# Kernel tuning notes

Hardware: AMD Instinct MI355X
Metric: run time of the kernel (lower is better)

The kernel has to match this reference:

```python
import jax, jax.numpy as jnp
import numpy as np

D_MODEL, N_HEADS, D_K, D_V, D_FF, SEQ = 2048, 16, 128, 128, 8192, 2048
EPS = 1e-5


def _layernorm(x, g, b):
    mu = jnp.mean(x, axis=-1, keepdims=True)
    var = jnp.var(x, axis=-1, keepdims=True)
    return (x - mu) * jax.lax.rsqrt(var + EPS) * g + b


def setup_inputs() -> dict:
    key = jax.random.key(0)
    ks = jax.random.split(key, 10)
    return {
        "x": jax.random.normal(ks[0], (SEQ, D_MODEL), jnp.float32),
        # per-head projections stacked over heads (matches num_heads separate DotProductAttention params)
        "wq": jax.random.normal(ks[1], (N_HEADS, D_MODEL, D_K), jnp.float32),
        "wk": jax.random.normal(ks[2], (N_HEADS, D_MODEL, D_K), jnp.float32),
        "wv": jax.random.normal(ks[3], (N_HEADS, D_MODEL, D_V), jnp.float32),
        "w_proj": jax.random.normal(ks[4], (N_HEADS * D_V, D_MODEL), jnp.float32),
        "g1": jnp.ones((D_MODEL,), jnp.float32),
        "b1": jnp.zeros((D_MODEL,), jnp.float32),
        "fc1_w": jax.random.normal(ks[5], (D_MODEL, D_FF), jnp.float32) * 0.02,
        "fc1_b": jnp.zeros((D_FF,), jnp.float32),
        "fc2_w": jax.random.normal(ks[6], (D_FF, D_MODEL), jnp.float32) * 0.02,
        "fc2_b": jnp.zeros((D_MODEL,), jnp.float32),
        "g2": jnp.ones((D_MODEL,), jnp.float32),
        "b2": jnp.zeros((D_MODEL,), jnp.float32),
    }


def reference(x, wq, wk, wv, w_proj, g1, b1, fc1_w, fc1_b, fc2_w, fc2_b, g2, b2):
    # multi-head attention (heads batched via einsum; same math as the per-head loop)
    q = jnp.einsum("sd,hdk->hsk", x, wq)
    k = jnp.einsum("sd,hdk->hsk", x, wk)
    v = jnp.einsum("sd,hdv->hsv", x, wv)
    scores = jnp.einsum("hsk,htk->hst", q, k) * (1.0 / np.sqrt(D_K))
    attn = jax.nn.softmax(scores, axis=-1)
    heads = jnp.einsum("hst,htv->hsv", attn, v)  # [H,S,Dv]
    concat = jnp.transpose(heads, (1, 0, 2)).reshape(SEQ, N_HEADS * D_V)
    attn_out = concat @ w_proj
    # residual + LayerNorm (dropout=0 -> identity)
    h = _layernorm(x + attn_out, g1, b1)
    # FFN with ReLU
    ff = jax.nn.relu(h @ fc1_w + fc1_b) @ fc2_w + fc2_b
    return _layernorm(h + ff, g2, b2)
```

## Files before the change

### kernel.cpp

```cpp
#include <hip/hip_runtime.h>


typedef __bf16 bf16;
typedef __attribute__((ext_vector_type(8))) __bf16 bf16x8;
typedef __attribute__((ext_vector_type(4))) __bf16 bf16x4;
typedef __attribute__((ext_vector_type(4))) float f32x4;

#define MFMA(a, b, c) __builtin_amdgcn_mfma_f32_16x16x32_bf16((a), (b), (c), 0, 0, 0)
#define NEG_INF (-3.402823466e38f)

__device__ __forceinline__ void cp16(void* lds, const void* g) {
  __builtin_amdgcn_global_load_lds(
      (const __attribute__((address_space(1))) unsigned int*)g,
      (__attribute__((address_space(3))) unsigned int*)lds, 16, 0, 0);
}

#define SBAR() __builtin_amdgcn_sched_barrier(0)
#define GBAR()                              \
  do {                                      \
    asm volatile("" ::: "memory");          \
    __builtin_amdgcn_s_barrier();           \
    asm volatile("" ::: "memory");          \
  } while (0)
#define LGKM0()                                         \
  do {                                                  \
    asm volatile("s_waitcnt lgkmcnt(0)" ::: "memory");  \
    __builtin_amdgcn_sched_barrier(0);                  \
  } while (0)
#define VMC6()                                          \
  do {                                                  \
    asm volatile("s_waitcnt vmcnt(6)" ::: "memory");    \
    __builtin_amdgcn_sched_barrier(0);                  \
  } while (0)


__global__ void k_split_x(const float* __restrict__ x, bf16* __restrict__ xh,
                          bf16* __restrict__ xl) {
  int i = blockIdx.x * 256 + threadIdx.x;
  f32x4 v = ((const f32x4*)x)[i];
  bf16x4 h, l;
#pragma unroll
  for (int j = 0; j < 4; ++j) {
    bf16 hi = (bf16)v[j];
    h[j] = hi;
    l[j] = (bf16)(v[j] - (float)hi);
  }
  ((bf16x4*)xh)[i] = h;
  ((bf16x4*)xl)[i] = l;
}

template <bool SPLIT>
__global__ void k_tcvt(const float* __restrict__ in, bf16* __restrict__ oh,
                       bf16* __restrict__ ol, int R, int C) {
  __shared__ float t[64][65];
  long zoff = (long)blockIdx.z * R * C;
  int c0 = blockIdx.x * 64, r0 = blockIdx.y * 64;
  int cc = threadIdx.x & 63, rr = threadIdx.x >> 6;
#pragma unroll
  for (int i = 0; i < 16; ++i) {
    int r = i * 4 + rr;
    t[r][cc] = in[zoff + (long)(r0 + r) * C + c0 + cc];
  }
  __syncthreads();
#pragma unroll
  for (int i = 0; i < 16; ++i) {
    int orow = i * 4 + rr;
    float v = t[cc][orow];
    long oidx = zoff + (long)(c0 + orow) * R + r0 + cc;
    bf16 hi = (bf16)v;
    oh[oidx] = hi;
    if (SPLIT) ol[oidx] = (bf16)(v - (float)hi);
  }
}

__global__ void k_combine4(const float* __restrict__ p, long pstr,
                           bf16* __restrict__ o) {
  int i = blockIdx.x * 256 + threadIdx.x;
  f32x4 v = ((const f32x4*)p)[i];
#pragma unroll
  for (int zz = 1; zz < 4; ++zz) v += ((const f32x4*)(p + zz * pstr))[i];
  bf16x4 ob;
#pragma unroll
  for (int j = 0; j < 4; ++j) ob[j] = (bf16)v[j];
  ((bf16x4*)o)[i] = ob;
}

template <int EPI>
__global__ __launch_bounds__(512, 1) void k_gemm8(
    const bf16* __restrict__ A, const bf16* __restrict__ B,
    float* __restrict__ Cf, bf16* __restrict__ Cb,
    const float* __restrict__ bias, int M, int N, int K, int nsplit) {
  __shared__ char lds[131072];
  const int tid = threadIdx.x, w = tid >> 6, l = tid & 63;
  const int l16 = l & 15, lg = l >> 4;
  const int wr = w >> 2, wc = w & 3;
  const long bm0 = (long)blockIdx.y * 256, bn0 = (long)blockIdx.x * 256;
  const int z = blockIdx.z;
  const int ksz = K / nsplit, kbeg = z * ksz;
  const int nt = ksz >> 6;
  const long lK = K;

  const int srow = w * 8 + (l >> 3);
  const int sslot = (l & 7) ^ (l >> 3);

  auto STAGE = [&](int bufp, int isB, int h, int tt) {
    int tc = tt < nt ? tt : nt - 1;
    char* dst = lds + bufp * 65536 + isB * 32768 + h * 16384 + w * 1024;
    const bf16* G = isB ? B : A;
    long r0 = (isB ? bn0 : bm0) + h * 128 + srow;
    const bf16* src = G + r0 * lK + kbeg + tc * 64 + sslot * 8;
    cp16(dst, src);
    cp16(dst + 8192, src + 64 * lK);
  };
  auto LDA = [&](int bufp, int mf, int ks) -> bf16x8 {
    int inrow = (mf & 3) * 32 + wr * 16 + l16;
    int byo = bufp * 65536 + (mf >> 2) * 16384 + inrow * 128 +
              ((((ks << 2) + lg) ^ (inrow & 7)) << 4);
    return *(const bf16x8*)(lds + byo);
  };
  auto LDB = [&](int bufp, int nf, int ks) -> bf16x8 {
    int inrow = (nf & 1) * 64 + wc * 16 + l16;
    int byo = bufp * 65536 + 32768 + (nf >> 1) * 16384 + inrow * 128 +
              ((((ks << 2) + lg) ^ (inrow & 7)) << 4);
    return *(const bf16x8*)(lds + byo);
  };

  f32x4 acc[8][4];
#pragma unroll
  for (int mf = 0; mf < 8; ++mf)
#pragma unroll
    for (int nf = 0; nf < 4; ++nf)
#pragma unroll
      for (int j = 0; j < 4; ++j) acc[mf][nf][j] = 0.f;

  STAGE(0, 0, 0, 0);
  STAGE(0, 1, 0, 0);
  STAGE(0, 0, 1, 0);
  STAGE(0, 1, 1, 0);
  STAGE(1, 1, 0, 1);
  STAGE(1, 0, 1, 1);
  STAGE(1, 1, 1, 1);
  SBAR();
  VMC6();
  GBAR();

  bf16x8 a[4][2], b[2][2];
  for (int t = 0; t < nt; ++t) {
    const int cb = t & 1, nb = cb ^ 1;
#pragma unroll
    for (int mf = 0; mf < 4; ++mf)
#pragma unroll
      for (int ks = 0; ks < 2; ++ks) a[mf][ks] = LDA(cb, mf, ks);
#pragma unroll
    for (int nf = 0; nf < 2; ++nf)
#pragma unroll
      for (int ks = 0; ks < 2; ++ks) b[nf][ks] = LDB(cb, nf, ks);
    STAGE(nb, 0, 0, t + 1);
    SBAR();
    GBAR();
    LGKM0();
    __builtin_amdgcn_s_setprio(1);
#pragma unroll
    for (int mf = 0; mf < 4; ++mf)
#pragma unroll
      for (int nf = 0; nf < 2; ++nf)
#pragma unroll
        for (int ks = 0; ks < 2; ++ks)
          acc[mf][nf] = MFMA(a[mf][ks], b[nf][ks], acc[mf][nf]);
    __builtin_amdgcn_s_setprio(0);
    GBAR();
#pragma unroll
    for (int mf = 0; mf < 4; ++mf)
#pragma unroll
      for (int ks = 0; ks < 2; ++ks) a[mf][ks] = LDA(cb, mf + 4, ks);
    STAGE(cb, 1, 0, t + 2);
    SBAR();
    GBAR();
    LGKM0();
    __builtin_amdgcn_s_setprio(1);
#pragma unroll
    for (int mf = 0; mf < 4; ++mf)
#pragma unroll
      for (int nf = 0; nf < 2; ++nf)
#pragma unroll
        for (int ks = 0; ks < 2; ++ks)
          acc[mf + 4][nf] = MFMA(a[mf][ks], b[nf][ks], acc[mf + 4][nf]);
    __builtin_amdgcn_s_setprio(0);
    GBAR();
#pragma unroll
    for (int nf = 0; nf < 2; ++nf)
#pragma unroll
      for (int ks = 0; ks < 2; ++ks) b[nf][ks] = LDB(cb, nf + 2, ks);
    GBAR();
    LGKM0();
    __builtin_amdgcn_s_setprio(1);
#pragma unroll
    for (int mf = 0; mf < 4; ++mf)
#pragma unroll
      for (int nf = 0; nf < 2; ++nf)
#pragma unroll
        for (int ks = 0; ks < 2; ++ks)
          acc[mf + 4][nf + 2] = MFMA(a[mf][ks], b[nf][ks], acc[mf + 4][nf + 2]);
    __builtin_amdgcn_s_setprio(0);
    GBAR();
#pragma unroll
    for (int mf = 0; mf < 4; ++mf)
#pragma unroll
      for (int ks = 0; ks < 2; ++ks) a[mf][ks] = LDA(cb, mf, ks);
    STAGE(cb, 0, 1, t + 2);
    STAGE(cb, 1, 1, t + 2);
    SBAR();
    VMC6();
    GBAR();
    LGKM0();
    __builtin_amdgcn_s_setprio(1);
#pragma unroll
    for (int mf = 0; mf < 4; ++mf)
#pragma unroll
      for (int nf = 0; nf < 2; ++nf)
#pragma unroll
        for (int ks = 0; ks < 2; ++ks)
          acc[mf][nf + 2] = MFMA(a[mf][ks], b[nf][ks], acc[mf][nf + 2]);
    __builtin_amdgcn_s_setprio(0);
    GBAR();
  }
  asm volatile("s_waitcnt vmcnt(0) lgkmcnt(0)" ::: "memory");

#pragma unroll
  for (int mf = 0; mf < 8; ++mf)
#pragma unroll
    for (int nf = 0; nf < 4; ++nf) {
      long col = bn0 + nf * 64 + wc * 16 + l16;
      float bv = (EPI == 2) ? bias[col] : 0.f;
#pragma unroll
      for (int jj = 0; jj < 4; ++jj) {
        long row = bm0 + mf * 32 + wr * 16 + lg * 4 + jj;
        float v = acc[mf][nf][jj];
        if (EPI == 0) {
          Cf[(long)z * M * N + row * N + col] = v;
        } else {
          v = fmaxf(v + bv, 0.f);
          Cb[row * N + col] = (bf16)v;
        }
      }
    }
}

__global__ __launch_bounds__(512, 1) void k_split8(
    const bf16* __restrict__ Ah_g, const bf16* __restrict__ Al_g,
    const bf16* __restrict__ Bh_g, const bf16* __restrict__ Bl_g,
    bf16* __restrict__ Ch, bf16* __restrict__ Cl,
    int M, int N, int K, float scale, int scale_ncols) {
  __shared__ char lds[98304];
  const int tid = threadIdx.x, w = tid >> 6, l = tid & 63;
  const int l16 = l & 15, lg = l >> 4;
  const int wr = w >> 2, wc = w & 3;
  const long bm0 = (long)blockIdx.y * 128, bn0 = (long)blockIdx.x * 256;
  const int nt = K >> 5;
  const long lK = K;

  const int srcrow = tid >> 2;
  const int ss = (tid & 3) ^ ((tid >> 3) & 3);

  auto STG_A = [&](int bufp, int isLo, int tt) {
    int tc = tt < nt ? tt : nt - 1;
    char* dst = lds + bufp * 49152 + isLo * 8192 + tid * 16;
    const bf16* G = isLo ? Al_g : Ah_g;
    cp16(dst, &G[(bm0 + srcrow) * lK + tc * 32 + ss * 8]);
  };
  auto STG_B = [&](int bufp, int isLo, int half, int tt) {
    int tc = tt < nt ? tt : nt - 1;
    char* dst = lds + bufp * 49152 + 16384 + isLo * 16384 + half * 8192 + tid * 16;
    const bf16* G = isLo ? Bl_g : Bh_g;
    cp16(dst, &G[(bn0 + half * 128 + srcrow) * lK + tc * 32 + ss * 8]);
  };
  auto LDA8 = [&](int bufp, int mf, int isLo) -> bf16x8 {
    int row = mf * 32 + wr * 16 + l16;
    int byo = bufp * 49152 + isLo * 8192 + row * 64 +
              ((lg ^ ((row >> 1) & 3)) << 4);
    return *(const bf16x8*)(lds + byo);
  };
  auto LDB8 = [&](int bufp, int nf, int isLo) -> bf16x8 {
    int row = nf * 64 + wc * 16 + l16;
    int byo = bufp * 49152 + 16384 + isLo * 16384 + row * 64 +
              ((lg ^ ((row >> 1) & 3)) << 4);
    return *(const bf16x8*)(lds + byo);
  };

  f32x4 acc[4][4];
#pragma unroll
  for (int mf = 0; mf < 4; ++mf)
#pragma unroll
    for (int nf = 0; nf < 4; ++nf)
#pragma unroll
      for (int j = 0; j < 4; ++j) acc[mf][nf][j] = 0.f;

  STG_B(0, 0, 0, 0); STG_B(0, 1, 0, 0);
  STG_A(0, 0, 0);    STG_A(0, 1, 0);
  STG_B(0, 0, 1, 0); STG_B(0, 1, 1, 0);
  STG_B(1, 0, 0, 1); STG_B(1, 1, 0, 1);
  STG_A(1, 0, 1);    STG_A(1, 1, 1);
  STG_B(1, 0, 1, 1); STG_B(1, 1, 1, 1);
  SBAR();
  VMC6();
  GBAR();

  bf16x8 ah[4], al[4], bh[2], bl[2];
  for (int t = 0; t < nt; ++t) {
    const int cb = t & 1;
#pragma unroll
    for (int mf = 0; mf < 2; ++mf) {
      ah[mf] = LDA8(cb, mf, 0);
      al[mf] = LDA8(cb, mf, 1);
    }
#pragma unroll
    for (int nf = 0; nf < 2; ++nf) {
      bh[nf] = LDB8(cb, nf, 0);
      bl[nf] = LDB8(cb, nf, 1);
    }
    SBAR();
    GBAR();
    LGKM0();
    __builtin_amdgcn_s_setprio(1);
#pragma unroll
    for (int mf = 0; mf < 2; ++mf)
#pragma unroll
      for (int nf = 0; nf < 2; ++nf) {
        acc[mf][nf] = MFMA(ah[mf], bh[nf], acc[mf][nf]);
        acc[mf][nf] = MFMA(ah[mf], bl[nf], acc[mf][nf]);
        acc[mf][nf] = MFMA(al[mf], bh[nf], acc[mf][nf]);
      }
    __builtin_amdgcn_s_setprio(0);
    GBAR();
#pragma unroll
    for (int mf = 2; mf < 4; ++mf) {
      ah[mf] = LDA8(cb, mf, 0);
      al[mf] = LDA8(cb, mf, 1);
    }
    STG_B(cb, 0, 0, t + 2);
    STG_B(cb, 1, 0, t + 2);
    SBAR();
    GBAR();
    LGKM0();
    __builtin_amdgcn_s_setprio(1);
#pragma unroll
    for (int mf = 2; mf < 4; ++mf)
#pragma unroll
      for (int nf = 0; nf < 2; ++nf) {
        acc[mf][nf] = MFMA(ah[mf], bh[nf], acc[mf][nf]);
        acc[mf][nf] = MFMA(ah[mf], bl[nf], acc[mf][nf]);
        acc[mf][nf] = MFMA(al[mf], bh[nf], acc[mf][nf]);
      }
    __builtin_amdgcn_s_setprio(0);
    GBAR();
#pragma unroll
    for (int nf = 0; nf < 2; ++nf) {
      bh[nf] = LDB8(cb, nf + 2, 0);
      bl[nf] = LDB8(cb, nf + 2, 1);
    }
    STG_A(cb, 0, t + 2);
    STG_A(cb, 1, t + 2);
    SBAR();
    GBAR();
    LGKM0();
    __builtin_amdgcn_s_setprio(1);
#pragma unroll
    for (int mf = 2; mf < 4; ++mf)
#pragma unroll
      for (int nf = 0; nf < 2; ++nf) {
        acc[mf][nf + 2] = MFMA(ah[mf], bh[nf], acc[mf][nf + 2]);
        acc[mf][nf + 2] = MFMA(ah[mf], bl[nf], acc[mf][nf + 2]);
        acc[mf][nf + 2] = MFMA(al[mf], bh[nf], acc[mf][nf + 2]);
      }
    __builtin_amdgcn_s_setprio(0);
    GBAR();
    STG_B(cb, 0, 1, t + 2);
    STG_B(cb, 1, 1, t + 2);
    SBAR();
    VMC6();
    GBAR();
    __builtin_amdgcn_s_setprio(1);
#pragma unroll
    for (int mf = 0; mf < 2; ++mf)
#pragma unroll
      for (int nf = 0; nf < 2; ++nf) {
        acc[mf][nf + 2] = MFMA(ah[mf], bh[nf], acc[mf][nf + 2]);
        acc[mf][nf + 2] = MFMA(ah[mf], bl[nf], acc[mf][nf + 2]);
        acc[mf][nf + 2] = MFMA(al[mf], bh[nf], acc[mf][nf + 2]);
      }
    __builtin_amdgcn_s_setprio(0);
    GBAR();
  }
  asm volatile("s_waitcnt vmcnt(0) lgkmcnt(0)" ::: "memory");

#pragma unroll
  for (int mf = 0; mf < 4; ++mf)
#pragma unroll
    for (int nf = 0; nf < 4; ++nf) {
      long col = bn0 + nf * 64 + wc * 16 + l16;
      float sc = (col < scale_ncols) ? scale : 1.0f;
#pragma unroll
      for (int j = 0; j < 4; ++j) {
        long row = bm0 + mf * 32 + wr * 16 + lg * 4 + j;
        float v = acc[mf][nf][j] * sc;
        bf16 hi = (bf16)v;
        Ch[row * N + col] = hi;
        Cl[row * N + col] = (bf16)(v - (float)hi);
      }
    }
}

__global__ __launch_bounds__(256, 3) void k_flash(
    const bf16* __restrict__ Qh, const bf16* __restrict__ Ql,
    const bf16* __restrict__ Kh, const bf16* __restrict__ Kl,
    const bf16* __restrict__ Vt, bf16* __restrict__ Oc) {
  __shared__ bf16 sm[24576];
  bf16* sKh = sm;
  bf16* sKl = sm + 8192;
  bf16* sVt = sm + 16384;
  bf16* sP = sKl;
  const int tid = threadIdx.x, w = tid >> 6, l = tid & 63;
  const int l16 = l & 15, lg = l >> 4;
  const int head = blockIdx.y;
  const long q0 = (long)blockIdx.x * 64;

  bf16x8 qh_r[4], ql_r[4];
#pragma unroll
  for (int kk = 0; kk < 4; ++kk) {
    long off = (q0 + w * 16 + l16) * 4096 + head * 128 + kk * 32 + lg * 8;
    qh_r[kk] = *(const bf16x8*)&Qh[off];
    ql_r[kk] = *(const bf16x8*)&Ql[off];
  }

  f32x4 acc_o[8];
#pragma unroll
  for (int n = 0; n < 8; ++n)
#pragma unroll
    for (int j = 0; j < 4; ++j) acc_o[n][j] = 0.f;
  float mrow[4], lrow[4];
#pragma unroll
  for (int j = 0; j < 4; ++j) {
    mrow[j] = NEG_INF;
    lrow[j] = 0.f;
  }

  for (int t0 = 0; t0 < 2048; t0 += 64) {
    __syncthreads();
#pragma unroll
    for (int i = 0; i < 4; ++i) {
      int c = (w * 4 + i) * 64 + l;
      int rk = c >> 4, sk = (c & 15) ^ (rk & 7);
      long ko = (long)(t0 + rk) * 4096 + head * 128 + sk * 8;
      int db = (w * 4 + i) * 512;
      cp16(&sKh[db], &Kh[ko]);
      cp16(&sKl[db], &Kl[ko]);
      int rv = c >> 3, sv = (c & 7) ^ (rv & 7);
      long vo = (long)(head * 128 + rv) * 2048 + t0 + sv * 8;
      cp16(&sVt[db], &Vt[vo]);
    }
    __syncthreads();

    f32x4 s[4];
#pragma unroll
    for (int n = 0; n < 4; ++n)
#pragma unroll
      for (int j = 0; j < 4; ++j) s[n][j] = 0.f;
    __builtin_amdgcn_s_setprio(1);
#pragma unroll
    for (int kk = 0; kk < 4; ++kk) {
      bf16x8 bh[4], bl[4];
#pragma unroll
      for (int n = 0; n < 4; ++n) {
        int r = n * 16 + l16;
        int byo = r * 256 + (((kk * 4 + lg) ^ (r & 7)) << 4);
        bh[n] = *(const bf16x8*)((const char*)sKh + byo);
        bl[n] = *(const bf16x8*)((const char*)sKl + byo);
      }
#pragma unroll
      for (int n = 0; n < 4; ++n) {
        s[n] = MFMA(qh_r[kk], bh[n], s[n]);
        s[n] = MFMA(qh_r[kk], bl[n], s[n]);
        s[n] = MFMA(ql_r[kk], bh[n], s[n]);
      }
    }
    __builtin_amdgcn_s_setprio(0);
    __syncthreads();

#pragma unroll
    for (int j = 0; j < 4; ++j) {
      float mx = fmaxf(fmaxf(s[0][j], s[1][j]), fmaxf(s[2][j], s[3][j]));
      mx = fmaxf(mx, __shfl_xor(mx, 1));
      mx = fmaxf(mx, __shfl_xor(mx, 2));
      mx = fmaxf(mx, __shfl_xor(mx, 4));
      mx = fmaxf(mx, __shfl_xor(mx, 8));
      float mo = mrow[j];
      float mn = fmaxf(mo, mx);
      mrow[j] = mn;
      float f = __expf(mo - mn);
      int prow = w * 16 + lg * 4 + j;
      float ssum = 0.f;
#pragma unroll
      for (int n = 0; n < 4; ++n) {
        float p = __expf(s[n][j] - mn);
        ssum += p;
        int byo = prow * 128 + (((n * 16 + l16) * 2) ^ ((prow & 7) << 4));
        *(bf16*)((char*)sP + byo) = (bf16)p;
      }
      ssum += __shfl_xor(ssum, 1);
      ssum += __shfl_xor(ssum, 2);
      ssum += __shfl_xor(ssum, 4);
      ssum += __shfl_xor(ssum, 8);
      lrow[j] = lrow[j] * f + ssum;
#pragma unroll
      for (int n = 0; n < 8; ++n) acc_o[n][j] *= f;
    }

    __builtin_amdgcn_s_setprio(1);
#pragma unroll
    for (int kk = 0; kk < 2; ++kk) {
      bf16x8 pa, bv[8];
      {
        int r = w * 16 + l16;
        int byo = r * 128 + (((kk * 4 + lg) ^ (r & 7)) << 4);
        pa = *(const bf16x8*)((const char*)sP + byo);
      }
#pragma unroll
      for (int n = 0; n < 8; ++n) {
        int r = n * 16 + l16;
        int byo = r * 128 + (((kk * 4 + lg) ^ (r & 7)) << 4);
        bv[n] = *(const bf16x8*)((const char*)sVt + byo);
      }
#pragma unroll
      for (int n = 0; n < 8; ++n) acc_o[n] = MFMA(pa, bv[n], acc_o[n]);
    }
    __builtin_amdgcn_s_setprio(0);
  }

#pragma unroll
  for (int j = 0; j < 4; ++j) {
    float rinv = 1.f / lrow[j];
    long row = q0 + w * 16 + lg * 4 + j;
#pragma unroll
    for (int n = 0; n < 8; ++n)
      Oc[row * 2048 + head * 128 + n * 16 + l16] = (bf16)(acc_o[n][j] * rinv);
  }
}

__global__ __launch_bounds__(256) void k_add_ln(
    const float* __restrict__ a, const float* __restrict__ p, long pstr,
    int np, const float* __restrict__ bias, const float* __restrict__ g,
    const float* __restrict__ be, float* __restrict__ o32,
    bf16* __restrict__ obf) {
  __shared__ float red[8];
  int row = blockIdx.x, tid = threadIdx.x;
  const float* pa = a + (long)row * 2048;
  f32x4 v[2];
  float sum = 0.f, sq = 0.f;
#pragma unroll
  for (int i = 0; i < 2; ++i) {
    int idx = i * 1024 + tid * 4;
    v[i] = *(const f32x4*)(pa + idx);
    for (int zz = 0; zz < np; ++zz)
      v[i] += *(const f32x4*)(p + zz * pstr + (long)row * 2048 + idx);
    if (bias != nullptr) v[i] += *(const f32x4*)(bias + idx);
#pragma unroll
    for (int j = 0; j < 4; ++j) {
      sum += v[i][j];
      sq += v[i][j] * v[i][j];
    }
  }
#pragma unroll
  for (int o = 1; o < 64; o <<= 1) {
    sum += __shfl_xor(sum, o);
    sq += __shfl_xor(sq, o);
  }
  int w = tid >> 6;
  if ((tid & 63) == 0) {
    red[w * 2] = sum;
    red[w * 2 + 1] = sq;
  }
  __syncthreads();
  sum = red[0] + red[2] + red[4] + red[6];
  sq = red[1] + red[3] + red[5] + red[7];
  float mu = sum * (1.f / 2048.f);
  float var = sq * (1.f / 2048.f) - mu * mu;
  float rs = rsqrtf(var + 1e-5f);
#pragma unroll
  for (int i = 0; i < 2; ++i) {
    int idx = i * 1024 + tid * 4;
    f32x4 vg = *(const f32x4*)(g + idx);
    f32x4 vb = *(const f32x4*)(be + idx);
    f32x4 o;
#pragma unroll
    for (int j = 0; j < 4; ++j) o[j] = (v[i][j] - mu) * rs * vg[j] + vb[j];
    *(f32x4*)(o32 + (long)row * 2048 + idx) = o;
    if (obf != nullptr) {
      bf16x4 ob;
#pragma unroll
      for (int j = 0; j < 4; ++j) ob[j] = (bf16)o[j];
      *(bf16x4*)(obf + (long)row * 2048 + idx) = ob;
    }
  }
}

extern "C" void kernel_launch(void* const* d_in, const int* in_sizes, int n_in,
                              void* d_out, int out_size, void* d_ws, size_t ws_size,
                              hipStream_t stream) {
  const float* x    = (const float*)d_in[0];
  const float* wq   = (const float*)d_in[1];
  const float* wk   = (const float*)d_in[2];
  const float* wv   = (const float*)d_in[3];
  const float* wp   = (const float*)d_in[4];
  const float* g1   = (const float*)d_in[5];
  const float* b1   = (const float*)d_in[6];
  const float* fc1w = (const float*)d_in[7];
  const float* fc1b = (const float*)d_in[8];
  const float* fc2w = (const float*)d_in[9];
  const float* fc2b = (const float*)d_in[10];
  const float* g2   = (const float*)d_in[11];
  const float* b2   = (const float*)d_in[12];
  float* out = (float*)d_out;

  char* ws = (char*)d_ws;
  const size_t MB = 1024 * 1024;
  if (ws_size < 216 * MB) return;
  const long W4M = 4L * 1024 * 1024;

  bf16* xh    = (bf16*)(ws + 0 * MB);
  bf16* xl    = (bf16*)(ws + 8 * MB);
  bf16* qk_bh = (bf16*)(ws + 16 * MB);
  bf16* qk_bl = (bf16*)(ws + 32 * MB);
  bf16* wvt   = (bf16*)(ws + 48 * MB);
  bf16* wpt   = (bf16*)(ws + 56 * MB);
  bf16* fc1t  = (bf16*)(ws + 64 * MB);
  bf16* fc2t  = (bf16*)(ws + 96 * MB);
  float* vtp  = (float*)(ws + 128 * MB);
  bf16* vtb   = (bf16*)(ws + 192 * MB);
  bf16* qkh   = (bf16*)(ws + 128 * MB);
  bf16* qkl   = (bf16*)(ws + 144 * MB);
  bf16* cc    = (bf16*)(ws + 200 * MB);
  float* aop  = (float*)(ws + 128 * MB);
  float* h32  = (float*)(ws + 192 * MB);
  bf16*  hbf  = (bf16*)(ws + 208 * MB);
  bf16*  ff1  = (bf16*)(ws + 128 * MB);
  float* ffp  = (float*)(ws + 0 * MB);
  const long PSTR = 4194304L;

  k_split_x<<<4096, 256, 0, stream>>>(x, xh, xl);
  k_tcvt<true ><<<dim3(2, 32, 16), 256, 0, stream>>>(wq, qk_bh, qk_bl, 2048, 128);
  k_tcvt<true ><<<dim3(2, 32, 16), 256, 0, stream>>>(wk, qk_bh + W4M, qk_bl + W4M,
                                                     2048, 128);
  k_tcvt<false><<<dim3(2, 32, 16), 256, 0, stream>>>(wv, wvt, nullptr, 2048, 128);
  k_tcvt<false><<<dim3(32, 32, 1), 256, 0, stream>>>(wp, wpt, nullptr, 2048, 2048);
  k_tcvt<false><<<dim3(128, 32, 1), 256, 0, stream>>>(fc1w, fc1t, nullptr, 2048, 8192);
  k_tcvt<false><<<dim3(32, 128, 1), 256, 0, stream>>>(fc2w, fc2t, nullptr, 8192, 2048);

  k_gemm8<0><<<dim3(8, 8, 4), 512, 0, stream>>>(
      wvt, xh, vtp, nullptr, nullptr, 2048, 2048, 2048, 4);
  k_combine4<<<4096, 256, 0, stream>>>(vtp, PSTR, vtb);
  k_split8<<<dim3(16, 16), 512, 0, stream>>>(
      xh, xl, qk_bh, qk_bl, qkh, qkl, 2048, 4096, 2048,
      0.08838834764831845f, 2048);
  k_flash<<<dim3(32, 16), 256, 0, stream>>>(qkh, qkl, qkh + 2048, qkl + 2048,
                                            vtb, cc);
  k_gemm8<0><<<dim3(8, 8, 4), 512, 0, stream>>>(
      cc, wpt, aop, nullptr, nullptr, 2048, 2048, 2048, 4);
  k_add_ln<<<2048, 256, 0, stream>>>(x, aop, PSTR, 4, nullptr, g1, b1, h32, hbf);
  k_gemm8<2><<<dim3(32, 8, 1), 512, 0, stream>>>(
      hbf, fc1t, nullptr, ff1, fc1b, 2048, 8192, 2048, 1);
  k_gemm8<0><<<dim3(8, 8, 4), 512, 0, stream>>>(
      ff1, fc2t, ffp, nullptr, nullptr, 2048, 2048, 8192, 4);
  k_add_ln<<<2048, 256, 0, stream>>>(h32, ffp, PSTR, 4, fc2b, g2, b2, out, nullptr);
}
```

Before: 515.7 us.

## Split flash attention over two KV halves with a separate combine kernel

```diff
diff --git a/kernel.cpp b/kernel.cpp
--- a/kernel.cpp
+++ b/kernel.cpp
@@ -83,6 +83,32 @@
 #pragma unroll
   for (int j = 0; j < 4; ++j) ob[j] = (bf16)v[j];
   ((bf16x4*)o)[i] = ob;
+}
+
+__global__ void k_fcomb(const float* __restrict__ op,
+                        const float* __restrict__ mb,
+                        const float* __restrict__ lb,
+                        bf16* __restrict__ cc) {
+  int row = blockIdx.x, tid = threadIdx.x;
+  int col = tid * 8;
+  int head = col >> 7;
+  float m1 = mb[head * 2048 + row], m2 = mb[32768 + head * 2048 + row];
+  float l1 = lb[head * 2048 + row], l2 = lb[32768 + head * 2048 + row];
+  float m = fmaxf(m1, m2);
+  float s1 = __expf(m1 - m), s2 = __expf(m2 - m);
+  float rinv = 1.f / (l1 * s1 + l2 * s2);
+  const float* o1 = op + (long)row * 2048 + col;
+  const float* o2 = o1 + 4194304L;
+  f32x4 a0 = *(const f32x4*)o1, a1 = *(const f32x4*)(o1 + 4);
+  f32x4 b0 = *(const f32x4*)o2, b1 = *(const f32x4*)(o2 + 4);
+  bf16x4 r0, r1;
+#pragma unroll
+  for (int j = 0; j < 4; ++j) {
+    r0[j] = (bf16)((a0[j] * s1 + b0[j] * s2) * rinv);
+    r1[j] = (bf16)((a1[j] * s1 + b1[j] * s2) * rinv);
+  }
+  *(bf16x4*)(cc + (long)row * 2048 + col) = r0;
+  *(bf16x4*)(cc + (long)row * 2048 + col + 4) = r1;
 }
 
 template <int EPI>
@@ -413,7 +439,8 @@
 __global__ __launch_bounds__(256, 3) void k_flash(
     const bf16* __restrict__ Qh, const bf16* __restrict__ Ql,
     const bf16* __restrict__ Kh, const bf16* __restrict__ Kl,
-    const bf16* __restrict__ Vt, bf16* __restrict__ Oc) {
+    const bf16* __restrict__ Vt, float* __restrict__ Op,
+    float* __restrict__ Mb, float* __restrict__ Lb) {
   __shared__ bf16 sm[24576];
   bf16* sKh = sm;
   bf16* sKl = sm + 8192;
@@ -423,6 +450,7 @@
   const int l16 = l & 15, lg = l >> 4;
   const int head = blockIdx.y;
   const long q0 = (long)blockIdx.x * 64;
+  const int kv0 = blockIdx.z * 1024;
 
   bf16x8 qh_r[4], ql_r[4];
 #pragma unroll
@@ -444,7 +472,7 @@
     lrow[j] = 0.f;
   }
 
-  for (int t0 = 0; t0 < 2048; t0 += 64) {
+  for (int t0 = kv0; t0 < kv0 + 1024; t0 += 64) {
     __syncthreads();
 #pragma unroll
     for (int i = 0; i < 4; ++i) {
@@ -536,13 +564,17 @@
     __builtin_amdgcn_s_setprio(0);
   }
 
+  const long zoff = (long)blockIdx.z * 4194304L;
 #pragma unroll
   for (int j = 0; j < 4; ++j) {
-    float rinv = 1.f / lrow[j];
     long row = q0 + w * 16 + lg * 4 + j;
 #pragma unroll
     for (int n = 0; n < 8; ++n)
-      Oc[row * 2048 + head * 128 + n * 16 + l16] = (bf16)(acc_o[n][j] * rinv);
+      Op[zoff + row * 2048 + head * 128 + n * 16 + l16] = acc_o[n][j];
+    if (l16 == 0) {
+      Mb[(blockIdx.z * 16 + head) * 2048 + row] = mrow[j];
+      Lb[(blockIdx.z * 16 + head) * 2048 + row] = lrow[j];
+    }
   }
 }
 
@@ -638,6 +670,9 @@
   bf16* vtb   = (bf16*)(ws + 192 * MB);
   bf16* qkh   = (bf16*)(ws + 128 * MB);
   bf16* qkl   = (bf16*)(ws + 144 * MB);
+  float* fop  = (float*)(ws + 0 * MB);
+  float* fmb  = (float*)(ws + 32 * MB);
+  float* flb  = (float*)(ws + 33 * MB);
   bf16* cc    = (bf16*)(ws + 200 * MB);
   float* aop  = (float*)(ws + 128 * MB);
   float* h32  = (float*)(ws + 192 * MB);
@@ -661,8 +696,9 @@
   k_split8<<<dim3(16, 16), 512, 0, stream>>>(
       xh, xl, qk_bh, qk_bl, qkh, qkl, 2048, 4096, 2048,
       0.08838834764831845f, 2048);
-  k_flash<<<dim3(32, 16), 256, 0, stream>>>(qkh, qkl, qkh + 2048, qkl + 2048,
-                                            vtb, cc);
+  k_flash<<<dim3(32, 16, 2), 256, 0, stream>>>(qkh, qkl, qkh + 2048, qkl + 2048,
+                                               vtb, fop, fmb, flb);
+  k_fcomb<<<2048, 256, 0, stream>>>(fop, fmb, flb, cc);
   k_gemm8<0><<<dim3(8, 8, 4), 512, 0, stream>>>(
       cc, wpt, aop, nullptr, nullptr, 2048, 2048, 2048, 4);
   k_add_ln<<<2048, 256, 0, stream>>>(x, aop, PSTR, 4, nullptr, g1, b1, h32, hbf);
```

New measurement: 531.8 us. 1.03x slower.

## Double-buffer K/V tiles in flash attention with 32-key blocks

Applied to the files above, without the earlier changes.

```diff
diff --git a/kernel.cpp b/kernel.cpp
--- a/kernel.cpp
+++ b/kernel.cpp
@@ -414,11 +414,8 @@
     const bf16* __restrict__ Qh, const bf16* __restrict__ Ql,
     const bf16* __restrict__ Kh, const bf16* __restrict__ Kl,
     const bf16* __restrict__ Vt, bf16* __restrict__ Oc) {
-  __shared__ bf16 sm[24576];
-  bf16* sKh = sm;
-  bf16* sKl = sm + 8192;
-  bf16* sVt = sm + 16384;
-  bf16* sP = sKl;
+  __shared__ bf16 sm[26624];
+  bf16* sP = sm + 24576;
   const int tid = threadIdx.x, w = tid >> 6, l = tid & 63;
   const int l16 = l & 15, lg = l >> 4;
   const int head = blockIdx.y;
@@ -432,6 +429,21 @@
     ql_r[kk] = *(const bf16x8*)&Ql[off];
   }
 
+  auto STAGE = [&](int buf, int kt) {
+    char* base = (char*)sm + buf * 24576;
+#pragma unroll
+    for (int i = 0; i < 2; ++i) {
+      int u = i * 256 + tid;
+      int rk = u >> 4, sk = (u & 15) ^ (rk & 7);
+      long ko = (long)(kt + rk) * 4096 + head * 128 + sk * 8;
+      cp16(base + u * 16, &Kh[ko]);
+      cp16(base + 8192 + u * 16, &Kl[ko]);
+      int rv = u >> 2, sv = (u & 3) ^ (rv & 3);
+      long vo = (long)(head * 128 + rv) * 2048 + kt + sv * 8;
+      cp16(base + 16384 + u * 16, &Vt[vo]);
+    }
+  };
+
   f32x4 acc_o[8];
 #pragma unroll
   for (int n = 0; n < 8; ++n)
@@ -444,51 +456,44 @@
     lrow[j] = 0.f;
   }
 
-  for (int t0 = 0; t0 < 2048; t0 += 64) {
-    __syncthreads();
-#pragma unroll
-    for (int i = 0; i < 4; ++i) {
-      int c = (w * 4 + i) * 64 + l;
-      int rk = c >> 4, sk = (c & 15) ^ (rk & 7);
-      long ko = (long)(t0 + rk) * 4096 + head * 128 + sk * 8;
-      int db = (w * 4 + i) * 512;
-      cp16(&sKh[db], &Kh[ko]);
-      cp16(&sKl[db], &Kl[ko]);
-      int rv = c >> 3, sv = (c & 7) ^ (rv & 7);
-      long vo = (long)(head * 128 + rv) * 2048 + t0 + sv * 8;
-      cp16(&sVt[db], &Vt[vo]);
-    }
-    __syncthreads();
-
-    f32x4 s[4];
-#pragma unroll
-    for (int n = 0; n < 4; ++n)
+  STAGE(0, 0);
+  STAGE(1, 32);
+  SBAR();
+  VMC6();
+  GBAR();
+
+  for (int t = 0; t < 64; ++t) {
+    const int cur = t & 1;
+    const char* kb = (const char*)sm + cur * 24576;
+
+    f32x4 s[2];
+#pragma unroll
+    for (int n = 0; n < 2; ++n)
 #pragma unroll
       for (int j = 0; j < 4; ++j) s[n][j] = 0.f;
     __builtin_amdgcn_s_setprio(1);
 #pragma unroll
     for (int kk = 0; kk < 4; ++kk) {
-      bf16x8 bh[4], bl[4];
-#pragma unroll
-      for (int n = 0; n < 4; ++n) {
+      bf16x8 bh[2], bl[2];
+#pragma unroll
+      for (int n = 0; n < 2; ++n) {
         int r = n * 16 + l16;
         int byo = r * 256 + (((kk * 4 + lg) ^ (r & 7)) << 4);
-        bh[n] = *(const bf16x8*)((const char*)sKh + byo);
-        bl[n] = *(const bf16x8*)((const char*)sKl + byo);
-      }
-#pragma unroll
-      for (int n = 0; n < 4; ++n) {
+        bh[n] = *(const bf16x8*)(kb + byo);
+        bl[n] = *(const bf16x8*)(kb + 8192 + byo);
+      }
+#pragma unroll
+      for (int n = 0; n < 2; ++n) {
         s[n] = MFMA(qh_r[kk], bh[n], s[n]);
         s[n] = MFMA(qh_r[kk], bl[n], s[n]);
         s[n] = MFMA(ql_r[kk], bh[n], s[n]);
       }
     }
     __builtin_amdgcn_s_setprio(0);
-    __syncthreads();
 
 #pragma unroll
     for (int j = 0; j < 4; ++j) {
-      float mx = fmaxf(fmaxf(s[0][j], s[1][j]), fmaxf(s[2][j], s[3][j]));
+      float mx = fmaxf(s[0][j], s[1][j]);
       mx = fmaxf(mx, __shfl_xor(mx, 1));
       mx = fmaxf(mx, __shfl_xor(mx, 2));
       mx = fmaxf(mx, __shfl_xor(mx, 4));
@@ -500,10 +505,10 @@
       int prow = w * 16 + lg * 4 + j;
       float ssum = 0.f;
 #pragma unroll
-      for (int n = 0; n < 4; ++n) {
+      for (int n = 0; n < 2; ++n) {
         float p = __expf(s[n][j] - mn);
         ssum += p;
-        int byo = prow * 128 + (((n * 16 + l16) * 2) ^ ((prow & 7) << 4));
+        int byo = prow * 64 + (((n * 16 + l16) * 2) ^ ((prow & 3) << 4));
         *(bf16*)((char*)sP + byo) = (bf16)p;
       }
       ssum += __shfl_xor(ssum, 1);
@@ -516,25 +521,30 @@
     }
 
     __builtin_amdgcn_s_setprio(1);
-#pragma unroll
-    for (int kk = 0; kk < 2; ++kk) {
-      bf16x8 pa, bv[8];
-      {
-        int r = w * 16 + l16;
-        int byo = r * 128 + (((kk * 4 + lg) ^ (r & 7)) << 4);
-        pa = *(const bf16x8*)((const char*)sP + byo);
-      }
-#pragma unroll
-      for (int n = 0; n < 8; ++n) {
-        int r = n * 16 + l16;
-        int byo = r * 128 + (((kk * 4 + lg) ^ (r & 7)) << 4);
-        bv[n] = *(const bf16x8*)((const char*)sVt + byo);
-      }
-#pragma unroll
-      for (int n = 0; n < 8; ++n) acc_o[n] = MFMA(pa, bv[n], acc_o[n]);
-    }
-    __builtin_amdgcn_s_setprio(0);
-  }
+    bf16x8 pa, bv[8];
+    {
+      int r = w * 16 + l16;
+      int byo = r * 64 + ((lg ^ (r & 3)) << 4);
+      pa = *(const bf16x8*)((const char*)sP + byo);
+    }
+#pragma unroll
+    for (int n = 0; n < 8; ++n) {
+      int r = n * 16 + l16;
+      int byo = r * 64 + ((lg ^ (r & 3)) << 4);
+      bv[n] = *(const bf16x8*)(kb + 16384 + byo);
+    }
+#pragma unroll
+    for (int n = 0; n < 8; ++n) acc_o[n] = MFMA(pa, bv[n], acc_o[n]);
+    __builtin_amdgcn_s_setprio(0);
+
+    GBAR();
+    int nkt = (t + 2 < 64) ? (t + 2) * 32 : t * 32;
+    STAGE(cur, nkt);
+    SBAR();
+    VMC6();
+    GBAR();
+  }
+  asm volatile("s_waitcnt vmcnt(0) lgkmcnt(0)" ::: "memory");
 
 #pragma unroll
   for (int j = 0; j < 4; ++j) {
```

New measurement: 551.0 us. 6.8% more time.
